# Optimization experiments

Measured on AMD Instinct MI355X. Metric: run time of the kernel, lower is better.

Reference implementation:

```python
import jax, jax.numpy as jnp
import numpy as np

EMBED_DIM = 1024
NUM_HEADS = 16
HEAD_DIM = EMBED_DIM // NUM_HEADS
NUM_GLOBAL = 2
NUM_RANDOM = 3
WINDOW_SIZE = 3
B, S = 2, 2048


def setup_inputs() -> dict:
    key = jax.random.key(0)
    ks = jax.random.split(key, 10)
    scale = 0.02
    inp = {
        "x": jax.random.normal(ks[0], (B, S, EMBED_DIM), dtype=jnp.float32),
        "random_indices": jax.random.randint(ks[1], (S, NUM_RANDOM), 0, S, dtype=jnp.int32),
        "q_w": jax.random.normal(ks[2], (EMBED_DIM, EMBED_DIM), dtype=jnp.float32) * scale,
        "q_b": jnp.zeros((EMBED_DIM,), dtype=jnp.float32),
        "k_w": jax.random.normal(ks[3], (EMBED_DIM, EMBED_DIM), dtype=jnp.float32) * scale,
        "k_b": jnp.zeros((EMBED_DIM,), dtype=jnp.float32),
        "v_w": jax.random.normal(ks[4], (EMBED_DIM, EMBED_DIM), dtype=jnp.float32) * scale,
        "v_b": jnp.zeros((EMBED_DIM,), dtype=jnp.float32),
        "o_w": jax.random.normal(ks[5], (EMBED_DIM, EMBED_DIM), dtype=jnp.float32) * scale,
        "o_b": jnp.zeros((EMBED_DIM,), dtype=jnp.float32),
    }
    return inp


def _build_mask(random_indices, seq_len):
    # [S, S] boolean BigBird mask: global rows/cols + sliding window + random.
    i = jnp.arange(seq_len)[:, None]
    j = jnp.arange(seq_len)[None, :]
    glob = (i < NUM_GLOBAL) | (j < NUM_GLOBAL)
    win = jnp.abs(i - j) <= WINDOW_SIZE
    rand = jnp.zeros((seq_len, seq_len), dtype=bool)
    rows = jnp.repeat(jnp.arange(seq_len), NUM_RANDOM)
    rand = rand.at[rows, random_indices.reshape(-1)].set(True)
    return glob | win | rand


def reference(x, random_indices, q_w, q_b, k_w, k_b, v_w, v_b, o_w, o_b):
    b, s, _ = x.shape
    # torch nn.Linear: y = x @ W.T + b
    q = (x @ q_w.T + q_b).reshape(b, s, NUM_HEADS, HEAD_DIM).transpose(0, 2, 1, 3)
    k = (x @ k_w.T + k_b).reshape(b, s, NUM_HEADS, HEAD_DIM).transpose(0, 2, 1, 3)
    v = (x @ v_w.T + v_b).reshape(b, s, NUM_HEADS, HEAD_DIM).transpose(0, 2, 1, 3)
    scores = jnp.einsum("bhqd,bhkd->bhqk", q, k) / jnp.sqrt(jnp.float32(HEAD_DIM))
    mask = _build_mask(random_indices, s)  # [S, S]
    scores = jnp.where(mask[None, None, :, :], scores, -jnp.inf)
    probs = jax.nn.softmax(scores, axis=-1)
    out = jnp.einsum("bhqk,bhkd->bhqd", probs, v)
    out = out.transpose(0, 2, 1, 3).reshape(b, s, EMBED_DIM)
    return out @ o_w.T + o_b
```

## Files before the change

kernel.cpp:

```cpp
#include <hip/hip_runtime.h>

#define B_  2
#define S_  2048
#define E_  1024
#define H_  16
#define D_  64
#define NGLOB 2
#define NRAND 3
#define WIN 3

typedef __bf16 bf16x8 __attribute__((ext_vector_type(8)));
typedef float  f32x4  __attribute__((ext_vector_type(4)));

__device__ __forceinline__ unsigned short f2bf(float f) {
    unsigned u = __builtin_bit_cast(unsigned, f);
    unsigned r = u + 0x7FFFu + ((u >> 16) & 1u);
    return (unsigned short)(r >> 16);
}
__device__ __forceinline__ float bf2f(unsigned short u) {
    return __builtin_bit_cast(float, (unsigned)u << 16);
}

__device__ __forceinline__ void g2l16(const unsigned short* g, unsigned short* l) {
    __builtin_amdgcn_global_load_lds(
        (const __attribute__((address_space(1))) unsigned*)g,
        (__attribute__((address_space(3))) unsigned*)l, 16, 0, 0);
}

__global__ __launch_bounds__(256)
void convert_all(const float* __restrict__ x,  const float* __restrict__ qw,
                 const float* __restrict__ kw, const float* __restrict__ vw,
                 const float* __restrict__ ow,
                 unsigned short* __restrict__ xb, unsigned short* __restrict__ wqkv,
                 unsigned short* __restrict__ wo) {
    const int XN = (B_ * S_ * E_) / 4;
    const int WN = (E_ * E_) / 4;
    int i = blockIdx.x * blockDim.x + threadIdx.x;
    int r, loc;
    if (i < XN) { r = 0; loc = i; }
    else        { int j = i - XN; r = 1 + (j >> 18); loc = j & (WN - 1); }
    const float* src = r == 0 ? x : r == 1 ? qw : r == 2 ? kw : r == 3 ? vw : ow;
    float4 f = ((const float4*)src)[loc];
    ushort4 u;
    u.x = f2bf(f.x); u.y = f2bf(f.y); u.z = f2bf(f.z); u.w = f2bf(f.w);
    ushort4* dst = r == 0 ? (ushort4*)xb : r == 4 ? (ushort4*)wo
                 : (ushort4*)wqkv + (size_t)(r - 1) * WN;
    dst[loc] = u;
}

__global__ __launch_bounds__(256, 3)
void gemm_qkv(const unsigned short* __restrict__ A,
              const unsigned short* __restrict__ W,
              const float* __restrict__ b0, const float* __restrict__ b1,
              const float* __restrict__ b2,
              unsigned short* __restrict__ Cb, int M, int N, int K) {
    __shared__ unsigned short sA[128 * 64];
    __shared__ unsigned short sB[128 * 64];
    const int t = threadIdx.x;
    const int lane = t & 63;
    const int wave = t >> 6;
    const int wm = wave >> 1, wn = wave & 1;
    const int lq = lane >> 4;
    const int lr = lane & 15;
    const int bm = blockIdx.x * 128;
    const int bn = blockIdx.y * 128;

    f32x4 acc[4][4] = {};

    for (int k0 = 0; k0 < K; k0 += 64) {
        const unsigned short* Abase = A + (size_t)bm * K + k0;
        const unsigned short* Wbase = W + (size_t)bn * K + k0;
        #pragma unroll
        for (int j = 0; j < 4; ++j) {
            int c = j * 256 + t;
            int row = c >> 3, cc = c & 7;
            int gcol = ((cc ^ (row & 7)) << 3);
            int dst = j * 2048 + wave * 512;
            g2l16(Abase + (size_t)row * K + gcol, sA + dst);
            g2l16(Wbase + (size_t)row * K + gcol, sB + dst);
        }
        __syncthreads();

        #pragma unroll
        for (int ks = 0; ks < 2; ++ks) {
            const int sw = (((ks << 2) + lq) ^ (lr & 7)) << 3;
            bf16x8 af[4], bfr[4];
            #pragma unroll
            for (int i = 0; i < 4; ++i)
                af[i] = *(const bf16x8*)&sA[(wm * 64 + i * 16 + lr) * 64 + sw];
            #pragma unroll
            for (int j = 0; j < 4; ++j)
                bfr[j] = *(const bf16x8*)&sB[(wn * 64 + j * 16 + lr) * 64 + sw];
            #pragma unroll
            for (int i = 0; i < 4; ++i)
                #pragma unroll
                for (int j = 0; j < 4; ++j)
                    acc[i][j] = __builtin_amdgcn_mfma_f32_16x16x32_bf16(af[i], bfr[j], acc[i][j], 0, 0, 0);
        }
        __syncthreads();
    }

    #pragma unroll
    for (int i = 0; i < 4; ++i) {
        int row0 = bm + wm * 64 + i * 16 + lq * 4;
        #pragma unroll
        for (int j = 0; j < 4; ++j) {
            int col = bn + wn * 64 + j * 16 + lr;
            const float* bp = col < E_ ? b0 : (col < 2 * E_ ? b1 : b2);
            float bv = bp[col & (E_ - 1)];
            #pragma unroll
            for (int r = 0; r < 4; ++r)
                Cb[(size_t)(row0 + r) * N + col] = f2bf(acc[i][j][r] + bv);
        }
    }
}

__global__ __launch_bounds__(256, 2)
void gemm_o64(const unsigned short* __restrict__ A,
              const unsigned short* __restrict__ W,
              const float* __restrict__ bias,
              float* __restrict__ Cf, int M, int N, int K) {
    __shared__ unsigned short sA[128 * 64];
    __shared__ unsigned short sB[64 * 64];
    const int t = threadIdx.x;
    const int lane = t & 63;
    const int wave = t >> 6;
    const int lq = lane >> 4;
    const int lr = lane & 15;
    const int bm = blockIdx.x * 128;
    const int bn = blockIdx.y * 64;

    f32x4 acc[2][4] = {};

    for (int k0 = 0; k0 < K; k0 += 64) {
        const unsigned short* Abase = A + (size_t)bm * K + k0;
        const unsigned short* Wbase = W + (size_t)bn * K + k0;
        #pragma unroll
        for (int j = 0; j < 4; ++j) {
            int c = j * 256 + t;
            int row = c >> 3, cc = c & 7;
            int gcol = ((cc ^ (row & 7)) << 3);
            int dst = j * 2048 + wave * 512;
            g2l16(Abase + (size_t)row * K + gcol, sA + dst);
        }
        #pragma unroll
        for (int j = 0; j < 2; ++j) {
            int c = j * 256 + t;
            int row = c >> 3, cc = c & 7;
            int gcol = ((cc ^ (row & 7)) << 3);
            int dst = j * 2048 + wave * 512;
            g2l16(Wbase + (size_t)row * K + gcol, sB + dst);
        }
        __syncthreads();

        #pragma unroll
        for (int ks = 0; ks < 2; ++ks) {
            const int sw = (((ks << 2) + lq) ^ (lr & 7)) << 3;
            bf16x8 af[2], bfr[4];
            #pragma unroll
            for (int i = 0; i < 2; ++i)
                af[i] = *(const bf16x8*)&sA[(wave * 32 + i * 16 + lr) * 64 + sw];
            #pragma unroll
            for (int j = 0; j < 4; ++j)
                bfr[j] = *(const bf16x8*)&sB[(j * 16 + lr) * 64 + sw];
            #pragma unroll
            for (int i = 0; i < 2; ++i)
                #pragma unroll
                for (int j = 0; j < 4; ++j)
                    acc[i][j] = __builtin_amdgcn_mfma_f32_16x16x32_bf16(af[i], bfr[j], acc[i][j], 0, 0, 0);
        }
        __syncthreads();
    }

    #pragma unroll
    for (int i = 0; i < 2; ++i) {
        int row0 = bm + wave * 32 + i * 16 + lq * 4;
        #pragma unroll
        for (int j = 0; j < 4; ++j) {
            int col = bn + j * 16 + lr;
            float bv = bias[col];
            #pragma unroll
            for (int r = 0; r < 4; ++r)
                Cf[(size_t)(row0 + r) * N + col] = acc[i][j][r] + bv;
        }
    }
}

__global__ __launch_bounds__(256)
void attn_fused(const unsigned short* __restrict__ qkv,
                const int* __restrict__ rnd,
                float* __restrict__ gaccp,
                unsigned short* __restrict__ attn) {
    const int NB = B_ * (S_ - 2);
    int t = threadIdx.x;

    if (blockIdx.x < 512) {
        int tup = blockIdx.x >> 3, seg = blockIdx.x & 7;
        int b = tup >> 5, i = (tup >> 4) & 1, h = tup & 15;
        int w = t >> 6, l = t & 63;
        __shared__ float qs[D_];
        __shared__ float pc[256];
        __shared__ float red[4];
        __shared__ float ov[4][D_];
        if (t < D_) qs[t] = bf2f(qkv[(size_t)(b * S_ + i) * 3072 + h * D_ + t]);
        __syncthreads();

        float vals[8];
        float m = -1e30f;
        #pragma unroll
        for (int kk = 0; kk < 8; ++kk) {
            int c = kk * 256 + t;
            const bf16x8* kp = (const bf16x8*)(qkv + (size_t)(b * S_ + c) * 3072 + E_ + h * D_);
            float s = 0.f;
            #pragma unroll
            for (int u = 0; u < 8; ++u) {
                bf16x8 kv = kp[u];
                #pragma unroll
                for (int j = 0; j < 8; ++j) s += qs[u * 8 + j] * (float)kv[j];
            }
            vals[kk] = s * 0.125f;
            m = fmaxf(m, vals[kk]);
        }
        #pragma unroll
        for (int o = 32; o; o >>= 1) m = fmaxf(m, __shfl_down(m, o));
        if (l == 0) red[w] = m;
        __syncthreads();
        m = fmaxf(fmaxf(red[0], red[1]), fmaxf(red[2], red[3]));
        __syncthreads();
        float sum = 0.f;
        #pragma unroll
        for (int kk = 0; kk < 8; ++kk) { float e = __expf(vals[kk] - m); vals[kk] = e; sum += e; }
        #pragma unroll
        for (int o = 32; o; o >>= 1) sum += __shfl_down(sum, o);
        if (l == 0) red[w] = sum;
        __syncthreads();
        float inv = 1.f / (red[0] + red[1] + red[2] + red[3]);
        pc[t] = vals[seg] * inv;
        __syncthreads();

        const unsigned short* vbase =
            qkv + (size_t)(b * S_ + seg * 256 + w * 64) * 3072 + 2 * E_ + h * D_ + l;
        const float* pw = pc + w * 64;
        float acc = 0.f;
        #pragma unroll 8
        for (int k = 0; k < 64; ++k)
            acc += pw[k] * bf2f(vbase[(size_t)k * 3072]);
        ov[w][l] = acc;
        __syncthreads();
        if (w == 0)
            gaccp[((size_t)tup * 8 + seg) * D_ + l] =
                ov[0][l] + ov[1][l] + ov[2][l] + ov[3][l];
        return;
    }

    int bb = blockIdx.x - 512;
    int bidx = (bb & 7) * 128 + (bb >> 3);
    int w = t >> 6, l = t & 63;
    int row = bidx * 4 + w;
    bool valid = row < NB;
    int b = row / (S_ - 2);
    int i = row % (S_ - 2) + 2;
    if (!valid) { b = 0; i = 2; }

    __shared__ int   cols_s[4][12];
    __shared__ int   ncol_sh[4];
    __shared__ float pr_s[4][16 * 13 + 3];

    const bf16x8* qp = (const bf16x8*)(qkv + (size_t)(b * S_ + i) * 3072);
    bf16x8 q0 = qp[l * 2], q1 = qp[l * 2 + 1];
    float qreg[16];
    #pragma unroll
    for (int j = 0; j < 8; ++j) { qreg[j] = (float)q0[j]; qreg[8 + j] = (float)q1[j]; }

    if (l == 0) {
        int* cols = cols_s[w];
        int n = 0;
        cols[n++] = 0; cols[n++] = 1;
        int lo = i - WIN; if (lo < NGLOB) lo = NGLOB;
        int hi = i + WIN; if (hi > S_ - 1) hi = S_ - 1;
        for (int j = lo; j <= hi; ++j) cols[n++] = j;
        for (int r = 0; r < NRAND; ++r) {
            int c = rnd[i * NRAND + r];
            bool dup = false;
            for (int q = 0; q < n; ++q) dup = dup || (cols[q] == c);
            if (!dup) cols[n++] = c;
        }
        ncol_sh[w] = n;
        for (int q = n; q < 12; ++q) cols[q] = 0;
    }
    __syncthreads();
    const int n = ncol_sh[w];
    const int h4 = l >> 2;

    float sco[12];
    #pragma unroll
    for (int c = 0; c < 12; ++c) {
        const bf16x8* kp = (const bf16x8*)(qkv + (size_t)(b * S_ + cols_s[w][c]) * 3072 + E_);
        bf16x8 k0 = kp[l * 2], k1 = kp[l * 2 + 1];
        float s = 0.f;
        #pragma unroll
        for (int j = 0; j < 8; ++j) s += qreg[j] * (float)k0[j] + qreg[8 + j] * (float)k1[j];
        s += __shfl_xor(s, 1);
        s += __shfl_xor(s, 2);
        sco[c] = (c < n) ? s * 0.125f : -1e30f;
    }

    if ((l & 3) == 0) {
        float m = -1e30f;
        #pragma unroll
        for (int c = 0; c < 12; ++c) m = fmaxf(m, sco[c]);
        float sum = 0.f;
        #pragma unroll
        for (int c = 0; c < 12; ++c) { float e = __expf(sco[c] - m); sco[c] = e; sum += e; }
        float inv = 1.f / sum;
        #pragma unroll
        for (int c = 0; c < 12; ++c) pr_s[w][h4 * 13 + c] = sco[c] * inv;
    }
    __syncthreads();

    float o[16] = {};
    #pragma unroll
    for (int c = 0; c < 12; ++c) {
        float p = pr_s[w][h4 * 13 + c];
        const bf16x8* vp = (const bf16x8*)(qkv + (size_t)(b * S_ + cols_s[w][c]) * 3072 + 2 * E_);
        bf16x8 v0 = vp[l * 2], v1 = vp[l * 2 + 1];
        #pragma unroll
        for (int j = 0; j < 8; ++j) { o[j] += p * (float)v0[j]; o[8 + j] += p * (float)v1[j]; }
    }

    if (valid) {
        ushort4 u0, u1, u2, u3;
        u0.x = f2bf(o[0]);  u0.y = f2bf(o[1]);  u0.z = f2bf(o[2]);  u0.w = f2bf(o[3]);
        u1.x = f2bf(o[4]);  u1.y = f2bf(o[5]);  u1.z = f2bf(o[6]);  u1.w = f2bf(o[7]);
        u2.x = f2bf(o[8]);  u2.y = f2bf(o[9]);  u2.z = f2bf(o[10]); u2.w = f2bf(o[11]);
        u3.x = f2bf(o[12]); u3.y = f2bf(o[13]); u3.z = f2bf(o[14]); u3.w = f2bf(o[15]);
        ushort4* op = (ushort4*)(attn + (size_t)(b * S_ + i) * E_ + l * 16);
        op[0] = u0; op[1] = u1; op[2] = u2; op[3] = u3;
    }
}

__global__ __launch_bounds__(256)
void gattn_fin(const float* __restrict__ gaccp, unsigned short* __restrict__ attn) {
    int gid = blockIdx.x * 256 + threadIdx.x;
    int tup = gid >> 6, d = gid & 63;
    int b = tup >> 5, i = (tup >> 4) & 1, h = tup & 15;
    float s = 0.f;
    #pragma unroll
    for (int seg = 0; seg < 8; ++seg) s += gaccp[((size_t)tup * 8 + seg) * D_ + d];
    attn[(size_t)(b * S_ + i) * E_ + h * D_ + d] = f2bf(s);
}

extern "C" void kernel_launch(void* const* d_in, const int* in_sizes, int n_in,
                              void* d_out, int out_size, void* d_ws, size_t ws_size,
                              hipStream_t stream) {
    const float* x   = (const float*)d_in[0];
    const int*   rnd = (const int*)d_in[1];
    const float* qw  = (const float*)d_in[2];
    const float* qb  = (const float*)d_in[3];
    const float* kw  = (const float*)d_in[4];
    const float* kb  = (const float*)d_in[5];
    const float* vw  = (const float*)d_in[6];
    const float* vb  = (const float*)d_in[7];
    const float* ow  = (const float*)d_in[8];
    const float* ob  = (const float*)d_in[9];
    float* out = (float*)d_out;

    char* ws = (char*)d_ws;
    unsigned short* xb    = (unsigned short*)(ws);
    unsigned short* wqkv  = (unsigned short*)(ws + 8388608);
    unsigned short* wo    = (unsigned short*)(ws + 14680064);
    unsigned short* qkv   = (unsigned short*)(ws + 16777216);
    unsigned short* attn  = (unsigned short*)(ws + 41943040);
    float*          gaccp = (float*)(ws);

    const int M = B_ * S_;

    {
        int total4 = (M * E_ + 4 * E_ * E_) / 4;
        convert_all<<<total4 / 256, 256, 0, stream>>>(x, qw, kw, vw, ow, xb, wqkv, wo);
    }

    {
        dim3 grid(M / 128, 3 * E_ / 128);
        gemm_qkv<<<grid, 256, 0, stream>>>(xb, wqkv, qb, kb, vb, qkv, M, 3 * E_, E_);
    }

    attn_fused<<<512 + 1024, 256, 0, stream>>>(qkv, rnd, gaccp, attn);

    gattn_fin<<<16, 256, 0, stream>>>(gaccp, attn);

    {
        dim3 grid(M / 128, E_ / 64);
        gemm_o64<<<grid, 256, 0, stream>>>(attn, wo, ob, out, M, E_, E_);
    }
}
```

Measured before the change: 185.6 us.

## Split global-row softmax per segment and merge partial max/sum in finalize

Each global-row attention block used to compute scores for all 2048 keys, redundantly across its 8 segment blocks, and keep only its own segment. Now each block computes only its 256 keys, with 8 lanes cooperating per key through coalesced vector loads and xor-shuffle reductions. It writes a per-segment max and sum, which the finalize kernel uses to rescale and combine the partial outputs in log-sum-exp fashion. This removes 8x redundant QK work and the strided per-thread key loads, at the cost of an extra small buffer and a little more math in the finalize step.

```diff
diff --git a/kernel.cpp b/kernel.cpp
--- a/kernel.cpp
+++ b/kernel.cpp
@@ -189,7 +189,7 @@
 __global__ __launch_bounds__(256)
 void attn_fused(const unsigned short* __restrict__ qkv,
                 const int* __restrict__ rnd,
-                float* __restrict__ gaccp,
+                float* __restrict__ gaccp, float* __restrict__ gms,
                 unsigned short* __restrict__ attn) {
     const int NB = B_ * (S_ - 2);
     int t = threadIdx.x;
@@ -198,49 +198,60 @@
         int tup = blockIdx.x >> 3, seg = blockIdx.x & 7;
         int b = tup >> 5, i = (tup >> 4) & 1, h = tup & 15;
         int w = t >> 6, l = t & 63;
-        __shared__ float qs[D_];
-        __shared__ float pc[256];
+        __shared__ float ps[256];
         __shared__ float red[4];
         __shared__ float ov[4][D_];
-        if (t < D_) qs[t] = bf2f(qkv[(size_t)(b * S_ + i) * 3072 + h * D_ + t]);
-        __syncthreads();
-
-        float vals[8];
-        float m = -1e30f;
-        #pragma unroll
-        for (int kk = 0; kk < 8; ++kk) {
-            int c = kk * 256 + t;
-            const bf16x8* kp = (const bf16x8*)(qkv + (size_t)(b * S_ + c) * 3072 + E_ + h * D_);
+
+        const bf16x8* qp = (const bf16x8*)(qkv + (size_t)(b * S_ + i) * 3072 + h * D_);
+        bf16x8 qv = qp[l & 7];
+        float qreg[8];
+        #pragma unroll
+        for (int j = 0; j < 8; ++j) qreg[j] = (float)qv[j];
+
+        const int key0 = seg * 256 + w * 64;
+        float sc[8];
+        #pragma unroll
+        for (int it = 0; it < 8; ++it) {
+            int key = key0 + it * 8 + (l >> 3);
+            const bf16x8* kp = (const bf16x8*)(qkv + (size_t)(b * S_ + key) * 3072 + E_ + h * D_);
+            bf16x8 kv = kp[l & 7];
             float s = 0.f;
             #pragma unroll
-            for (int u = 0; u < 8; ++u) {
-                bf16x8 kv = kp[u];
-                #pragma unroll
-                for (int j = 0; j < 8; ++j) s += qs[u * 8 + j] * (float)kv[j];
-            }
-            vals[kk] = s * 0.125f;
-            m = fmaxf(m, vals[kk]);
-        }
-        #pragma unroll
-        for (int o = 32; o; o >>= 1) m = fmaxf(m, __shfl_down(m, o));
+            for (int j = 0; j < 8; ++j) s += qreg[j] * (float)kv[j];
+            s += __shfl_xor(s, 1);
+            s += __shfl_xor(s, 2);
+            s += __shfl_xor(s, 4);
+            sc[it] = s * 0.125f;
+        }
+        #pragma unroll
+        for (int it = 0; it < 8; ++it)
+            if ((l & 7) == 0) ps[w * 64 + it * 8 + (l >> 3)] = sc[it];
+        __syncthreads();
+
+        float v = ps[t];
+        float m = v;
+        #pragma unroll
+        for (int o = 32; o; o >>= 1) m = fmaxf(m, __shfl_xor(m, o));
         if (l == 0) red[w] = m;
         __syncthreads();
         m = fmaxf(fmaxf(red[0], red[1]), fmaxf(red[2], red[3]));
-        __syncthreads();
-        float sum = 0.f;
-        #pragma unroll
-        for (int kk = 0; kk < 8; ++kk) { float e = __expf(vals[kk] - m); vals[kk] = e; sum += e; }
-        #pragma unroll
-        for (int o = 32; o; o >>= 1) sum += __shfl_down(sum, o);
+        float e = __expf(v - m);
+        float sum = e;
+        #pragma unroll
+        for (int o = 32; o; o >>= 1) sum += __shfl_xor(sum, o);
+        __syncthreads();
         if (l == 0) red[w] = sum;
-        __syncthreads();
-        float inv = 1.f / (red[0] + red[1] + red[2] + red[3]);
-        pc[t] = vals[seg] * inv;
-        __syncthreads();
+        ps[t] = e;
+        __syncthreads();
+        if (t == 0) {
+            float stot = red[0] + red[1] + red[2] + red[3];
+            gms[(tup * 8 + seg) * 2]     = m;
+            gms[(tup * 8 + seg) * 2 + 1] = stot;
+        }
 
         const unsigned short* vbase =
-            qkv + (size_t)(b * S_ + seg * 256 + w * 64) * 3072 + 2 * E_ + h * D_ + l;
-        const float* pw = pc + w * 64;
+            qkv + (size_t)(b * S_ + key0) * 3072 + 2 * E_ + h * D_ + l;
+        const float* pw = ps + w * 64;
         float acc = 0.f;
         #pragma unroll 8
         for (int k = 0; k < 64; ++k)
@@ -340,14 +351,26 @@
 }
 
 __global__ __launch_bounds__(256)
-void gattn_fin(const float* __restrict__ gaccp, unsigned short* __restrict__ attn) {
+void gattn_fin(const float* __restrict__ gaccp, const float* __restrict__ gms,
+               unsigned short* __restrict__ attn) {
     int gid = blockIdx.x * 256 + threadIdx.x;
     int tup = gid >> 6, d = gid & 63;
     int b = tup >> 5, i = (tup >> 4) & 1, h = tup & 15;
-    float s = 0.f;
-    #pragma unroll
-    for (int seg = 0; seg < 8; ++seg) s += gaccp[((size_t)tup * 8 + seg) * D_ + d];
-    attn[(size_t)(b * S_ + i) * E_ + h * D_ + d] = f2bf(s);
+    float mc[8], sc[8], M = -1e30f;
+    #pragma unroll
+    for (int c = 0; c < 8; ++c) {
+        mc[c] = gms[(tup * 8 + c) * 2];
+        sc[c] = gms[(tup * 8 + c) * 2 + 1];
+        M = fmaxf(M, mc[c]);
+    }
+    float den = 0.f, num = 0.f;
+    #pragma unroll
+    for (int c = 0; c < 8; ++c) {
+        float f = __expf(mc[c] - M);
+        den += sc[c] * f;
+        num += gaccp[((size_t)tup * 8 + c) * D_ + d] * f;
+    }
+    attn[(size_t)(b * S_ + i) * E_ + h * D_ + d] = f2bf(num / den);
 }
 
 extern "C" void kernel_launch(void* const* d_in, const int* in_sizes, int n_in,
@@ -372,6 +395,7 @@
     unsigned short* qkv   = (unsigned short*)(ws + 16777216);
     unsigned short* attn  = (unsigned short*)(ws + 41943040);
     float*          gaccp = (float*)(ws);
+    float*          gms   = (float*)(ws + 131072);
 
     const int M = B_ * S_;
 
@@ -385,9 +409,9 @@
         gemm_qkv<<<grid, 256, 0, stream>>>(xb, wqkv, qb, kb, vb, qkv, M, 3 * E_, E_);
     }
 
-    attn_fused<<<512 + 1024, 256, 0, stream>>>(qkv, rnd, gaccp, attn);
-
-    gattn_fin<<<16, 256, 0, stream>>>(gaccp, attn);
+    attn_fused<<<512 + 1024, 256, 0, stream>>>(qkv, rnd, gaccp, gms, attn);
+
+    gattn_fin<<<16, 256, 0, stream>>>(gaccp, gms, attn);
 
     {
         dim3 grid(M / 128, E_ / 64);
```

New measurement: 167.3 us. -9.8%, faster.
